# Kernel optimization log

Hardware: AMD Instinct MI355X
Metric: run time of the kernel (lower is better)

Reference implementation:

```python
import jax, jax.numpy as jnp
import numpy as np


def setup_inputs() -> dict:
    key = jax.random.key(0)
    ks = jax.random.split(key, 11)
    B, E, R, D = 2048, 20000, 500, 256
    inp = {
        "h": jax.random.uniform(ks[0], (B, E), dtype=jnp.float32),
        "t": jax.random.uniform(ks[1], (B, E), dtype=jnp.float32),
        "r": jax.random.uniform(ks[2], (B, R), dtype=jnp.float32),
        "W_er": jax.random.normal(ks[3], (D, E), dtype=jnp.float32) * 0.02,
        "W_ei": jax.random.normal(ks[4], (D, E), dtype=jnp.float32) * 0.02,
        "W_ej": jax.random.normal(ks[5], (D, E), dtype=jnp.float32) * 0.02,
        "W_ek": jax.random.normal(ks[6], (D, E), dtype=jnp.float32) * 0.02,
        "W_rr": jax.random.normal(ks[7], (D, R), dtype=jnp.float32) * 0.02,
        "W_ri": jax.random.normal(ks[8], (D, R), dtype=jnp.float32) * 0.02,
        "W_rj": jax.random.normal(ks[9], (D, R), dtype=jnp.float32) * 0.02,
        "W_rk": jax.random.normal(ks[10], (D, R), dtype=jnp.float32) * 0.02,
    }
    return inp


def reference(h, t, r, W_er, W_ei, W_ej, W_ek, W_rr, W_ri, W_rj, W_rk):
    # entity / relation projections (nn.Linear, no bias): x @ W^T -> [B, D]
    H_r, H_i, H_j, H_k = h @ W_er.T, h @ W_ei.T, h @ W_ej.T, h @ W_ek.T
    T_r, T_i, T_j, T_k = t @ W_er.T, t @ W_ei.T, t @ W_ej.T, t @ W_ek.T
    R_r, R_i, R_j, R_k = r @ W_rr.T, r @ W_ri.T, r @ W_rj.T, r @ W_rk.T

    # hypercomplex norm per row: sqrt(|R_r|^2 + |R_i|^2 + |R_j|^2 + |R_k|^2) -> [B,1]
    norm = jnp.sqrt(
        jnp.sum(R_r * R_r + R_i * R_i + R_j * R_j + R_k * R_k, axis=1, keepdims=True)
    )
    R_r, R_i, R_j, R_k = norm * R_r, norm * R_i, norm * R_j, norm * R_k

    # Hamilton product H (x) R
    Q_r = H_r * R_r - H_i * R_i - H_j * R_j - H_k * R_k
    Q_i = H_r * R_i + H_i * R_r + H_j * R_k - H_k * R_j
    Q_j = H_r * R_j - H_i * R_k + H_j * R_r + H_k * R_i
    Q_k = H_r * R_k + H_i * R_j - H_j * R_i + H_k * R_r

    # diag(Q @ T^T) == rowwise dot sum(Q*T, axis=1) -- O(B*d) form of the anti-pattern
    score = jnp.sum(Q_r * T_r + Q_i * T_i + Q_j * T_j + Q_k * T_k, axis=1, keepdims=True)
    return jax.nn.sigmoid(score)
```

## Files before the change

### kernel.cpp

```cpp
#include <hip/hip_runtime.h>


using bf16x8 = __attribute__((ext_vector_type(8))) short;
using f32x4  = __attribute__((ext_vector_type(4))) float;
using f32x16 = __attribute__((ext_vector_type(16))) float;

#define DEVINL static __device__ __forceinline__

DEVINL void split2(float x0, float x1, unsigned& h, unsigned& l) {
  unsigned u0 = __float_as_uint(x0), u1 = __float_as_uint(x1);
  unsigned h0 = u0 & 0xFFFF0000u, h1 = u1 & 0xFFFF0000u;
  h = (u0 >> 16) | h1;
  float r0 = x0 - __uint_as_float(h0);
  float r1 = x1 - __uint_as_float(h1);
  l = (__float_as_uint(r0) >> 16) | (__float_as_uint(r1) & 0xFFFF0000u);
}

DEVINL void gload16(const void* g, void* l) {
  __builtin_amdgcn_global_load_lds(
      (const __attribute__((address_space(1))) unsigned*)g,
      (__attribute__((address_space(3))) unsigned*)l, 16, 0, 0);
}

__global__ void convert_img128(const float* __restrict__ src0,
                               const float* __restrict__ src1, int rows0,
                               int srcK, char* __restrict__ dst, int ktiles)
{
  __shared__ float ld[64][36];
  const int kt = blockIdx.x, rb = blockIdx.y;
  const int t = threadIdx.x;

  {
    int r = t >> 2, kc = (t & 3) * 8;
    int row = rb * 64 + r;
    const float* srow = (row < rows0) ? (src0 + (size_t)row * srcK)
                                      : (src1 + (size_t)(row - rows0) * srcK);
    int k0 = kt * 32 + kc;
    float4 v0, v1;
    if (k0 + 8 <= srcK) {
      v0 = *(const float4*)(srow + k0);
      v1 = *(const float4*)(srow + k0 + 4);
    } else {
      float x[8];
#pragma unroll
      for (int j = 0; j < 8; ++j) x[j] = (k0 + j < srcK) ? srow[k0 + j] : 0.f;
      v0 = make_float4(x[0], x[1], x[2], x[3]);
      v1 = make_float4(x[4], x[5], x[6], x[7]);
    }
    *(float4*)&ld[r][kc]     = v0;
    *(float4*)&ld[r][kc + 4] = v1;
  }
  __syncthreads();

  {
    int g = t >> 7, s = (t >> 6) & 1, kh = (t >> 5) & 1, r31 = t & 31;
    int row = g * 32 + r31;
    int k = s * 16 + kh * 8;
    float x[8];
#pragma unroll
    for (int j = 0; j < 8; ++j) x[j] = ld[row][k + j];
    unsigned hh[4], llv[4];
    split2(x[0], x[1], hh[0], llv[0]);
    split2(x[2], x[3], hh[1], llv[1]);
    split2(x[4], x[5], hh[2], llv[2]);
    split2(x[6], x[7], hh[3], llv[3]);
    int tile_rt = rb >> 1;
    int gbase = (rb & 1) * 2;
    char* base = dst + ((size_t)tile_rt * ktiles + kt) * 16384
               + (gbase + g) * 2048 + s * 1024 + kh * 512 + r31 * 16;
    *(uint4*)base          = make_uint4(hh[0], hh[1], hh[2], hh[3]);
    *(uint4*)(base + 8192) = make_uint4(llv[0], llv[1], llv[2], llv[3]);
  }
}

__global__ __launch_bounds__(256, 2) void gemm_t128(
    const char* __restrict__ Aimg, const char* __restrict__ Bimg, int ktiles,
    float* __restrict__ C, int MT, int NT, int KS, int swz)
{
  __shared__ __align__(16) char smem[65536];
  const int bid = blockIdx.x;

  int mt, nt, ks;
  if (swz) {
    int x = bid & 7, i = bid >> 3;
    nt = i & 7;
    int P = x * 8 + (i >> 3);
    ks = P & 1; mt = P >> 1;
  } else {
    nt = bid % NT; int q = bid / NT; mt = q % MT; ks = q / MT;
  }

  const int kt0 = (ktiles * ks) / KS;
  const int kt1 = (ktiles * (ks + 1)) / KS;

  const char* Ab = Aimg + ((size_t)mt * ktiles + kt0) * 16384;
  const char* Bb = Bimg + ((size_t)nt * ktiles + kt0) * 16384;

  const int wid = threadIdx.x >> 6, lane = threadIdx.x & 63;
  const int wr = wid >> 1, wc = wid & 1;

  f32x16 acc[2][2];
#pragma unroll
  for (int mb = 0; mb < 2; ++mb)
#pragma unroll
    for (int nb = 0; nb < 2; ++nb)
#pragma unroll
      for (int e = 0; e < 16; ++e) acc[mb][nb][e] = 0.f;

  {
    const char* As = Ab + wid * 4096 + lane * 16;
    const char* Bs = Bb + wid * 4096 + lane * 16;
#pragma unroll
    for (int i = 0; i < 4; ++i) gload16(As + i * 1024, smem + wid * 4096 + i * 1024);
#pragma unroll
    for (int i = 0; i < 4; ++i) gload16(Bs + i * 1024, smem + 16384 + wid * 4096 + i * 1024);
  }
  asm volatile("s_waitcnt vmcnt(0)" ::: "memory");
  __builtin_amdgcn_s_barrier();

  for (int kt = kt0; kt < kt1; ++kt) {
    char* bufc = smem + (size_t)((kt - kt0) & 1) * 32768;
    char* bufn = smem + (size_t)(((kt - kt0) & 1) ^ 1) * 32768;
    const bool nx = (kt + 1 < kt1);

    if (nx) {
      const char* As = Ab + (size_t)(kt + 1 - kt0) * 16384 + wid * 4096 + lane * 16;
      const char* Bs = Bb + (size_t)(kt + 1 - kt0) * 16384 + wid * 4096 + lane * 16;
#pragma unroll
      for (int i = 0; i < 4; ++i) gload16(As + i * 1024, bufn + wid * 4096 + i * 1024);
#pragma unroll
      for (int i = 0; i < 4; ++i) gload16(Bs + i * 1024, bufn + 16384 + wid * 4096 + i * 1024);
    }

    bf16x8 ah[2][2], al[2][2], bh[2][2], bl[2][2];
#pragma unroll
    for (int mb = 0; mb < 2; ++mb)
#pragma unroll
      for (int s = 0; s < 2; ++s) {
        const char* p = bufc + (wr * 2 + mb) * 2048 + s * 1024 + lane * 16;
        ah[mb][s] = *(const bf16x8*)p;
        al[mb][s] = *(const bf16x8*)(p + 8192);
      }
#pragma unroll
    for (int nb = 0; nb < 2; ++nb)
#pragma unroll
      for (int s = 0; s < 2; ++s) {
        const char* p = bufc + 16384 + (wc * 2 + nb) * 2048 + s * 1024 + lane * 16;
        bh[nb][s] = *(const bf16x8*)p;
        bl[nb][s] = *(const bf16x8*)(p + 8192);
      }

    __builtin_amdgcn_s_setprio(1);
#pragma unroll
    for (int p = 0; p < 3; ++p)
#pragma unroll
      for (int s = 0; s < 2; ++s)
#pragma unroll
        for (int mb = 0; mb < 2; ++mb)
#pragma unroll
          for (int nb = 0; nb < 2; ++nb) {
            bf16x8 av = (p == 1) ? al[mb][s] : ah[mb][s];
            bf16x8 bv = (p == 2) ? bl[nb][s] : bh[nb][s];
            acc[mb][nb] = __builtin_amdgcn_mfma_f32_32x32x16_bf16(av, bv, acc[mb][nb], 0, 0, 0);
          }
    __builtin_amdgcn_s_setprio(0);

    asm volatile("s_waitcnt vmcnt(0)" ::: "memory");
    __builtin_amdgcn_s_barrier();
  }

  float* Cb = C + (size_t)ks * (size_t)(MT * 128) * 1024;
  const long rowbase = (long)mt * 128 + wr * 64 + 4 * (lane >> 5);
  const long colbase = (long)nt * 128 + wc * 64 + (lane & 31);
#pragma unroll
  for (int mb = 0; mb < 2; ++mb)
#pragma unroll
    for (int nb = 0; nb < 2; ++nb)
#pragma unroll
      for (int reg = 0; reg < 16; ++reg) {
        long row = rowbase + mb * 32 + (reg & 3) + 8 * (reg >> 2);
        long col = colbase + nb * 32;
        Cb[(size_t)row * 1024 + col] = acc[mb][nb][reg];
      }
}

__global__ void convert_b16(const float* __restrict__ src, int srcK,
                            char* __restrict__ dst)
{
  const int tile = blockIdx.x;
  const int wrow = threadIdx.x;
  char* base = dst + (size_t)tile * 32768;
  const float* srow = src + (size_t)wrow * srcK;
#pragma unroll
  for (int kc8 = 0; kc8 < 4; ++kc8) {
    int k0 = tile * 32 + kc8 * 8;
    float x[8];
    if (k0 + 8 <= srcK) {
      float4 v0 = *(const float4*)(srow + k0);
      float4 v1 = *(const float4*)(srow + k0 + 4);
      x[0] = v0.x; x[1] = v0.y; x[2] = v0.z; x[3] = v0.w;
      x[4] = v1.x; x[5] = v1.y; x[6] = v1.z; x[7] = v1.w;
    } else {
#pragma unroll
      for (int j = 0; j < 8; ++j) x[j] = (k0 + j < srcK) ? srow[k0 + j] : 0.f;
    }
    unsigned hh[4], ll[4];
    split2(x[0], x[1], hh[0], ll[0]);
    split2(x[2], x[3], hh[1], ll[1]);
    split2(x[4], x[5], hh[2], ll[2]);
    split2(x[6], x[7], hh[3], ll[3]);
    int lchunk = (wrow & 15) + kc8 * 16;
    int n16 = wrow >> 4;
    *(uint4*)(base + (size_t)n16 * 1024 + lchunk * 16)         = make_uint4(hh[0], hh[1], hh[2], hh[3]);
    *(uint4*)(base + 16384 + (size_t)n16 * 1024 + lchunk * 16) = make_uint4(ll[0], ll[1], ll[2], ll[3]);
  }
}

__global__ void pad_r(const float* __restrict__ src, float* __restrict__ dst)
{
  int row = blockIdx.y;
  int k = threadIdx.x * 4;
  float4 v = make_float4(0.f, 0.f, 0.f, 0.f);
  if (k + 3 < 500) v = *(const float4*)(src + (size_t)row * 500 + k);
  *(float4*)(dst + (size_t)row * 512 + k) = v;
}

__global__ __launch_bounds__(512, 2) void gemm3p(
    const float* __restrict__ A0, const float* __restrict__ A1, int mtA0, long lda,
    const char* __restrict__ Bimg, int ktilesTot,
    float* __restrict__ C, long ldc, int MT, int NT, int KS, int swz)
{
  extern __shared__ char smemd[];
  const int tid = threadIdx.x;
  const int bid = blockIdx.x;

  int mt, nt, ks;
  if (swz) {
    int x = bid & 7, w = bid >> 3;
    nt = w & 3;
    int g = x + (w >> 2) * 8;
    mt = g & 15; ks = g >> 4;
  } else {
    nt = bid % NT; int q = bid / NT; mt = q % MT; ks = q / MT;
  }

  const int kt0 = (ktilesTot * ks) / KS;
  const int kt1 = (ktilesTot * (ks + 1)) / KS;

  const float* Ablk = (mt < mtA0) ? (A0 + (size_t)mt * 256 * lda)
                                  : (A1 + (size_t)(mt - mtA0) * 256 * lda);
  const char* Bt = Bimg + ((size_t)nt * ktilesTot + kt0) * 32768;

  const int wid = tid >> 6, lane = tid & 63;
  const int wr = wid >> 2, wc = wid & 3;
  const int l15 = lane & 15, lq = lane >> 4;

  const float* aSrc = Ablk + (size_t)(wid * 32 + (lane >> 3)) * lda
                      + (size_t)kt0 * 32 + 4 * (lane & 7);

  int awoff[4];
  {
    int kg = (lane & 7) >> 1, half = lane & 1;
#pragma unroll
    for (int i = 0; i < 4; ++i) {
      int m15 = (lane >> 3) + 8 * (i & 1);
      awoff[i] = (2 * wid + (i >> 1)) * 2048 + (((m15 ^ kg) + kg * 16) << 4) + half * 8;
    }
  }
  const int aroff = (((l15 ^ lq) + lq * 16) << 4);
  const int bbase = 32768 + (wc * 4) * 1024 + lane * 16;

  f32x4 acc[8][4];
#pragma unroll
  for (int m = 0; m < 8; ++m)
#pragma unroll
    for (int j = 0; j < 4; ++j)
#pragma unroll
      for (int e = 0; e < 4; ++e) acc[m][j][e] = 0.f;

  float4 aR[4];

#define ISSUE_A(KT)                                                            \
  {                                                                            \
    const float* p_ = aSrc + (size_t)((KT) - kt0) * 32;                        \
    _Pragma("unroll")                                                          \
    for (int i = 0; i < 4; ++i) aR[i] = *(const float4*)(p_ + (size_t)(8 * i) * lda); \
  }
#define ISSUE_B(DST, KT)                                                       \
  {                                                                            \
    const char* p_ = Bt + (size_t)((KT) - kt0) * 32768 + wid * 4096 + lane * 16; \
    _Pragma("unroll")                                                          \
    for (int i = 0; i < 4; ++i)                                                \
      gload16(p_ + i * 1024, (DST) + 32768 + wid * 4096 + i * 1024);           \
  }
#define WRITE_A(DST)                                                           \
  {                                                                            \
    _Pragma("unroll")                                                          \
    for (int i = 0; i < 4; ++i) {                                              \
      unsigned h0_, l0_, h1_, l1_;                                             \
      split2(aR[i].x, aR[i].y, h0_, l0_);                                      \
      split2(aR[i].z, aR[i].w, h1_, l1_);                                      \
      *(uint2*)((DST) + awoff[i])        = make_uint2(h0_, h1_);               \
      *(uint2*)((DST) + awoff[i] + 1024) = make_uint2(l0_, l1_);               \
    }                                                                          \
  }

  ISSUE_A(kt0);
  ISSUE_B(smemd, kt0);
  WRITE_A(smemd);
  asm volatile("s_waitcnt vmcnt(0)" ::: "memory");
  asm volatile("s_waitcnt lgkmcnt(0)" ::: "memory");
  __builtin_amdgcn_s_barrier();

  for (int kt = kt0; kt < kt1; ++kt) {
    char* bufc = smemd + (size_t)((kt - kt0) & 1) * 65536;
    char* bufn = smemd + (size_t)(((kt - kt0) & 1) ^ 1) * 65536;
    const bool nx = (kt + 1 < kt1);

    if (nx) { ISSUE_A(kt + 1); ISSUE_B(bufn, kt + 1); }

    bf16x8 bh[4], bl[4];
#pragma unroll
    for (int j = 0; j < 4; ++j) {
      bh[j] = *(const bf16x8*)(bufc + bbase + j * 1024);
      bl[j] = *(const bf16x8*)(bufc + bbase + j * 1024 + 16384);
    }

    __builtin_amdgcn_s_setprio(1);
#pragma unroll
    for (int m = 0; m < 4; ++m) {
      const char* ab = bufc + (wr * 8 + m) * 2048;
      bf16x8 ah = *(const bf16x8*)(ab + aroff);
      bf16x8 al = *(const bf16x8*)(ab + aroff + 1024);
#pragma unroll
      for (int j = 0; j < 4; ++j) {
        acc[m][j] = __builtin_amdgcn_mfma_f32_16x16x32_bf16(ah, bh[j], acc[m][j], 0, 0, 0);
        acc[m][j] = __builtin_amdgcn_mfma_f32_16x16x32_bf16(al, bh[j], acc[m][j], 0, 0, 0);
        acc[m][j] = __builtin_amdgcn_mfma_f32_16x16x32_bf16(ah, bl[j], acc[m][j], 0, 0, 0);
      }
    }
    __builtin_amdgcn_s_setprio(0);

    __builtin_amdgcn_sched_barrier(0);
    if (nx) WRITE_A(bufn);

    __builtin_amdgcn_s_setprio(1);
#pragma unroll
    for (int m = 4; m < 8; ++m) {
      const char* ab = bufc + (wr * 8 + m) * 2048;
      bf16x8 ah = *(const bf16x8*)(ab + aroff);
      bf16x8 al = *(const bf16x8*)(ab + aroff + 1024);
#pragma unroll
      for (int j = 0; j < 4; ++j) {
        acc[m][j] = __builtin_amdgcn_mfma_f32_16x16x32_bf16(ah, bh[j], acc[m][j], 0, 0, 0);
        acc[m][j] = __builtin_amdgcn_mfma_f32_16x16x32_bf16(al, bh[j], acc[m][j], 0, 0, 0);
        acc[m][j] = __builtin_amdgcn_mfma_f32_16x16x32_bf16(ah, bl[j], acc[m][j], 0, 0, 0);
      }
    }
    __builtin_amdgcn_s_setprio(0);

    asm volatile("s_waitcnt vmcnt(0)" ::: "memory");
    asm volatile("s_waitcnt lgkmcnt(0)" ::: "memory");
    __builtin_amdgcn_s_barrier();
  }
#undef ISSUE_A
#undef ISSUE_B
#undef WRITE_A

  float* Cb = C + (size_t)ks * (size_t)(MT * 256) * (size_t)ldc;
  const long rowbase = (long)mt * 256 + wr * 128 + lq * 4;
  const long colbase = (long)nt * 256 + wc * 64 + l15;
#pragma unroll
  for (int m = 0; m < 8; ++m)
#pragma unroll
    for (int j = 0; j < 4; ++j)
#pragma unroll
      for (int reg = 0; reg < 4; ++reg) {
        long row = rowbase + m * 16 + reg;
        long col = colbase + j * 16;
        Cb[(size_t)row * ldc + col] = acc[m][j][reg];
      }
}

__global__ void epilogue_kernel(const float* __restrict__ C1, const float* __restrict__ C2,
                                float* __restrict__ out, int KS)
{
  const int b = blockIdx.x;
  const int d = threadIdx.x;
  const size_t SZ = 4096ull * 1024ull;

  float Hq[4], Tq[4], Rq[4];
#pragma unroll
  for (int q = 0; q < 4; ++q) {
    float hv = 0.f, tv = 0.f;
    for (int ks = 0; ks < KS; ++ks) {
      hv += C1[ks * SZ + (size_t)b * 1024 + q * 256 + d];
      tv += C1[ks * SZ + (size_t)(b + 2048) * 1024 + q * 256 + d];
    }
    Hq[q] = hv; Tq[q] = tv;
    Rq[q] = C2[(size_t)b * 1024 + q * 256 + d];
  }
  float nn = Rq[0]*Rq[0] + Rq[1]*Rq[1] + Rq[2]*Rq[2] + Rq[3]*Rq[3];
  float Qr = Hq[0]*Rq[0] - Hq[1]*Rq[1] - Hq[2]*Rq[2] - Hq[3]*Rq[3];
  float Qi = Hq[0]*Rq[1] + Hq[1]*Rq[0] + Hq[2]*Rq[3] - Hq[3]*Rq[2];
  float Qj = Hq[0]*Rq[2] - Hq[1]*Rq[3] + Hq[2]*Rq[0] + Hq[3]*Rq[1];
  float Qk = Hq[0]*Rq[3] + Hq[1]*Rq[2] - Hq[2]*Rq[1] + Hq[3]*Rq[0];
  float ss = Qr*Tq[0] + Qi*Tq[1] + Qj*Tq[2] + Qk*Tq[3];

#pragma unroll
  for (int o = 32; o; o >>= 1) {
    ss += __shfl_xor(ss, o);
    nn += __shfl_xor(nn, o);
  }
  __shared__ float red[8];
  int lane = d & 63, w = d >> 6;
  if (lane == 0) { red[w] = ss; red[4 + w] = nn; }
  __syncthreads();
  if (d == 0) {
    float S = red[0] + red[1] + red[2] + red[3];
    float N = red[4] + red[5] + red[6] + red[7];
    float score = sqrtf(N) * S;
    out[b] = 1.f / (1.f + expf(-score));
  }
}

extern "C" void kernel_launch(void* const* d_in, const int* in_sizes, int n_in,
                              void* d_out, int out_size, void* d_ws, size_t ws_size,
                              hipStream_t stream)
{
  const float* h = (const float*)d_in[0];
  const float* t = (const float*)d_in[1];
  const float* r = (const float*)d_in[2];
  const float* We[4] = {(const float*)d_in[3], (const float*)d_in[4],
                        (const float*)d_in[5], (const float*)d_in[6]};
  const float* Wr[4] = {(const float*)d_in[7], (const float*)d_in[8],
                        (const float*)d_in[9], (const float*)d_in[10]};
  float* out = (float*)d_out;
  char* ws = (char*)d_ws;

  const size_t offA  = 0;
  const size_t offB  = 327680000;
  const size_t offWr = offB + 81920000;
  const size_t offRi = offWr + 2097152;
  const size_t offC1 = offRi + 4194304;
  const size_t C1sz  = 4096ull * 1024ull * 4ull;
  const size_t offC2 = offC1 + 2 * C1sz;
  const size_t needImg = offC2 + 8388608;

  if (ws_size >= needImg) {
    float* C1 = (float*)(ws + offC1);
    float* C2 = (float*)(ws + offC2);

    convert_img128<<<dim3(625, 64), 256, 0, stream>>>(h, t, 2048, 20000, ws + offA, 625);
    for (int q = 0; q < 4; ++q) {
      convert_img128<<<dim3(625, 4), 256, 0, stream>>>(
          We[q], We[q], 2048, 20000, ws + offB + (size_t)q * 2 * 625 * 16384, 625);
      convert_img128<<<dim3(16, 4), 256, 0, stream>>>(
          Wr[q], Wr[q], 2048, 500, ws + offWr + (size_t)q * 2 * 16 * 16384, 16);
    }
    convert_img128<<<dim3(16, 32), 256, 0, stream>>>(r, r, 2048, 500, ws + offRi, 16);

    gemm_t128<<<dim3(512), 256, 0, stream>>>(
        ws + offA, ws + offB, 625, C1, 32, 8, 2, 1);
    gemm_t128<<<dim3(128), 256, 0, stream>>>(
        ws + offRi, ws + offWr, 16, C2, 16, 8, 1, 0);

    epilogue_kernel<<<dim3(2048), 256, 0, stream>>>(C1, C2, out, 2);
    return;
  }

  const size_t fB  = 0;
  const size_t fWr = 81920000;
  const size_t fR  = fWr + 2097152;
  const size_t fC1 = fR + 4194304;
  const int KS = (ws_size >= fC1 + 4 * C1sz + 8388608ull) ? 4 : 2;
  const size_t fC2 = fC1 + (size_t)KS * C1sz;

  float* rpad = (float*)(ws + fR);
  float* C1   = (float*)(ws + fC1);
  float* C2   = (float*)(ws + fC2);

  for (int q = 0; q < 4; ++q) {
    convert_b16<<<dim3(625), 256, 0, stream>>>(We[q], 20000, ws + fB + (size_t)q * 625 * 32768);
    convert_b16<<<dim3(16), 256, 0, stream>>>(Wr[q], 500, ws + fWr + (size_t)q * 16 * 32768);
  }
  pad_r<<<dim3(1, 2048), 128, 0, stream>>>(r, rpad);

  gemm3p<<<dim3(16 * 4 * KS), 512, 131072, stream>>>(
      h, t, 8, 20000L, (const char*)(ws + fB), 625,
      C1, 1024L, 16, 4, KS, KS == 4 ? 1 : 0);
  gemm3p<<<dim3(32), 512, 131072, stream>>>(
      rpad, rpad, 8, 512L, (const char*)(ws + fWr), 16,
      C2, 1024L, 8, 4, 1, 0);

  epilogue_kernel<<<dim3(2048), 256, 0, stream>>>(C1, C2, out, KS);
}
```

Measured before the change: 616.1 us.

## Enlarge GEMM block tile to 256x256 with split-K of four

The bf16 hi/lo split-precision GEMM now uses 256x256 output tiles per block instead of 128x128. Each wave holds a 4x4 grid of 32x32 accumulators and B fragments are double-buffered in registers across the nb loop. The packed image layout and the convert kernel change to match, and split-K goes from 2 to 4, giving 256 blocks. The larger tile raises arithmetic intensity and cuts global/LDS traffic per FLOP, at the cost of one block per CU (128KB LDS, many registers) and twice the partial-sum memory read back by the epilogue.

Result: slower. 633.8 us (+2.9%).

```diff
diff --git a/kernel.cpp b/kernel.cpp
--- a/kernel.cpp
+++ b/kernel.cpp
@@ -22,9 +22,9 @@
       (__attribute__((address_space(3))) unsigned*)l, 16, 0, 0);
 }
 
-__global__ void convert_img128(const float* __restrict__ src0,
-                               const float* __restrict__ src1, int rows0,
-                               int srcK, char* __restrict__ dst, int ktiles)
+__global__ void convert_img2(const float* __restrict__ src0,
+                             const float* __restrict__ src1, int rows0,
+                             int srcK, char* __restrict__ dst, int ktiles)
 {
   __shared__ float ld[64][36];
   const int kt = blockIdx.x, rb = blockIdx.y;
@@ -64,28 +64,28 @@
     split2(x[2], x[3], hh[1], llv[1]);
     split2(x[4], x[5], hh[2], llv[2]);
     split2(x[6], x[7], hh[3], llv[3]);
-    int tile_rt = rb >> 1;
-    int gbase = (rb & 1) * 2;
-    char* base = dst + ((size_t)tile_rt * ktiles + kt) * 16384
+    int tile_rt = rb >> 2;
+    int gbase = (rb & 3) * 2;
+    char* base = dst + ((size_t)tile_rt * ktiles + kt) * 32768
                + (gbase + g) * 2048 + s * 1024 + kh * 512 + r31 * 16;
-    *(uint4*)base          = make_uint4(hh[0], hh[1], hh[2], hh[3]);
-    *(uint4*)(base + 8192) = make_uint4(llv[0], llv[1], llv[2], llv[3]);
-  }
-}
-
-__global__ __launch_bounds__(256, 2) void gemm_t128(
+    *(uint4*)base           = make_uint4(hh[0], hh[1], hh[2], hh[3]);
+    *(uint4*)(base + 16384) = make_uint4(llv[0], llv[1], llv[2], llv[3]);
+  }
+}
+
+__global__ __launch_bounds__(256, 1) void gemm_fat(
     const char* __restrict__ Aimg, const char* __restrict__ Bimg, int ktiles,
     float* __restrict__ C, int MT, int NT, int KS, int swz)
 {
-  __shared__ __align__(16) char smem[65536];
+  __shared__ __align__(16) char smem[131072];
   const int bid = blockIdx.x;
 
   int mt, nt, ks;
   if (swz) {
-    int x = bid & 7, i = bid >> 3;
-    nt = i & 7;
-    int P = x * 8 + (i >> 3);
-    ks = P & 1; mt = P >> 1;
+    int x = bid & 7, w = bid >> 3;
+    nt = w & 3;
+    int g = x + (w >> 2) * 8;
+    mt = g & 15; ks = g >> 4;
   } else {
     nt = bid % NT; int q = bid / NT; mt = q % MT; ks = q / MT;
   }
@@ -93,89 +93,99 @@
   const int kt0 = (ktiles * ks) / KS;
   const int kt1 = (ktiles * (ks + 1)) / KS;
 
-  const char* Ab = Aimg + ((size_t)mt * ktiles + kt0) * 16384;
-  const char* Bb = Bimg + ((size_t)nt * ktiles + kt0) * 16384;
+  const char* Ab = Aimg + ((size_t)mt * ktiles + kt0) * 32768;
+  const char* Bb = Bimg + ((size_t)nt * ktiles + kt0) * 32768;
 
   const int wid = threadIdx.x >> 6, lane = threadIdx.x & 63;
   const int wr = wid >> 1, wc = wid & 1;
 
-  f32x16 acc[2][2];
-#pragma unroll
-  for (int mb = 0; mb < 2; ++mb)
-#pragma unroll
-    for (int nb = 0; nb < 2; ++nb)
+  f32x16 acc[4][4];
+#pragma unroll
+  for (int mb = 0; mb < 4; ++mb)
+#pragma unroll
+    for (int nb = 0; nb < 4; ++nb)
 #pragma unroll
       for (int e = 0; e < 16; ++e) acc[mb][nb][e] = 0.f;
 
-  {
-    const char* As = Ab + wid * 4096 + lane * 16;
-    const char* Bs = Bb + wid * 4096 + lane * 16;
-#pragma unroll
-    for (int i = 0; i < 4; ++i) gload16(As + i * 1024, smem + wid * 4096 + i * 1024);
-#pragma unroll
-    for (int i = 0; i < 4; ++i) gload16(Bs + i * 1024, smem + 16384 + wid * 4096 + i * 1024);
-  }
+  auto stage = [&](char* buf, size_t tOff) {
+    const char* src = (wid < 2) ? (Ab + tOff + (size_t)wid * 16384)
+                                : (Bb + tOff + (size_t)(wid - 2) * 16384);
+    char* dst = buf + wid * 16384;
+#pragma unroll
+    for (int i = 0; i < 16; ++i)
+      gload16(src + i * 1024 + lane * 16, dst + i * 1024);
+  };
+
+  stage(smem, 0);
   asm volatile("s_waitcnt vmcnt(0)" ::: "memory");
   __builtin_amdgcn_s_barrier();
 
+  const int abase = wr * 4 * 2048 + lane * 16;
+  const int bbase = 32768 + wc * 4 * 2048 + lane * 16;
+
   for (int kt = kt0; kt < kt1; ++kt) {
-    char* bufc = smem + (size_t)((kt - kt0) & 1) * 32768;
-    char* bufn = smem + (size_t)(((kt - kt0) & 1) ^ 1) * 32768;
+    char* bufc = smem + (size_t)((kt - kt0) & 1) * 65536;
+    char* bufn = smem + (size_t)(((kt - kt0) & 1) ^ 1) * 65536;
     const bool nx = (kt + 1 < kt1);
 
-    if (nx) {
-      const char* As = Ab + (size_t)(kt + 1 - kt0) * 16384 + wid * 4096 + lane * 16;
-      const char* Bs = Bb + (size_t)(kt + 1 - kt0) * 16384 + wid * 4096 + lane * 16;
-#pragma unroll
-      for (int i = 0; i < 4; ++i) gload16(As + i * 1024, bufn + wid * 4096 + i * 1024);
-#pragma unroll
-      for (int i = 0; i < 4; ++i) gload16(Bs + i * 1024, bufn + 16384 + wid * 4096 + i * 1024);
-    }
-
-    bf16x8 ah[2][2], al[2][2], bh[2][2], bl[2][2];
-#pragma unroll
-    for (int mb = 0; mb < 2; ++mb)
+    if (nx) stage(bufn, (size_t)(kt + 1 - kt0) * 32768);
+
+    bf16x8 ah[4][2], al[4][2];
+#pragma unroll
+    for (int mb = 0; mb < 4; ++mb)
 #pragma unroll
       for (int s = 0; s < 2; ++s) {
-        const char* p = bufc + (wr * 2 + mb) * 2048 + s * 1024 + lane * 16;
+        const char* p = bufc + abase + mb * 2048 + s * 1024;
         ah[mb][s] = *(const bf16x8*)p;
-        al[mb][s] = *(const bf16x8*)(p + 8192);
+        al[mb][s] = *(const bf16x8*)(p + 16384);
       }
-#pragma unroll
-    for (int nb = 0; nb < 2; ++nb)
-#pragma unroll
-      for (int s = 0; s < 2; ++s) {
-        const char* p = bufc + 16384 + (wc * 2 + nb) * 2048 + s * 1024 + lane * 16;
-        bh[nb][s] = *(const bf16x8*)p;
-        bl[nb][s] = *(const bf16x8*)(p + 8192);
+
+    bf16x8 bh[2][2], bl[2][2];
+#pragma unroll
+    for (int s = 0; s < 2; ++s) {
+      const char* p = bufc + bbase + s * 1024;
+      bh[0][s] = *(const bf16x8*)p;
+      bl[0][s] = *(const bf16x8*)(p + 16384);
+    }
+
+#pragma unroll
+    for (int nb = 0; nb < 4; ++nb) {
+      const int cur = nb & 1, nxt = cur ^ 1;
+      if (nb < 3) {
+#pragma unroll
+        for (int s = 0; s < 2; ++s) {
+          const char* p = bufc + bbase + (nb + 1) * 2048 + s * 1024;
+          bh[nxt][s] = *(const bf16x8*)p;
+          bl[nxt][s] = *(const bf16x8*)(p + 16384);
+        }
       }
-
-    __builtin_amdgcn_s_setprio(1);
-#pragma unroll
-    for (int p = 0; p < 3; ++p)
+      __builtin_amdgcn_sched_barrier(0);
+      __builtin_amdgcn_s_setprio(1);
 #pragma unroll
       for (int s = 0; s < 2; ++s)
 #pragma unroll
-        for (int mb = 0; mb < 2; ++mb)
-#pragma unroll
-          for (int nb = 0; nb < 2; ++nb) {
+        for (int p = 0; p < 3; ++p)
+#pragma unroll
+          for (int mb = 0; mb < 4; ++mb) {
             bf16x8 av = (p == 1) ? al[mb][s] : ah[mb][s];
-            bf16x8 bv = (p == 2) ? bl[nb][s] : bh[nb][s];
+            bf16x8 bv = (p == 2) ? bl[cur][s] : bh[cur][s];
             acc[mb][nb] = __builtin_amdgcn_mfma_f32_32x32x16_bf16(av, bv, acc[mb][nb], 0, 0, 0);
           }
-    __builtin_amdgcn_s_setprio(0);
+      __builtin_amdgcn_s_setprio(0);
+      __builtin_amdgcn_sched_barrier(0);
+    }
 
     asm volatile("s_waitcnt vmcnt(0)" ::: "memory");
     __builtin_amdgcn_s_barrier();
   }
 
-  float* Cb = C + (size_t)ks * (size_t)(MT * 128) * 1024;
-  const long rowbase = (long)mt * 128 + wr * 64 + 4 * (lane >> 5);
-  const long colbase = (long)nt * 128 + wc * 64 + (lane & 31);
-#pragma unroll
-  for (int mb = 0; mb < 2; ++mb)
-#pragma unroll
-    for (int nb = 0; nb < 2; ++nb)
+  float* Cb = C + (size_t)ks * (size_t)(MT * 256) * 1024;
+  const long rowbase = (long)mt * 256 + wr * 128 + 4 * (lane >> 5);
+  const long colbase = (long)nt * 256 + wc * 128 + (lane & 31);
+#pragma unroll
+  for (int mb = 0; mb < 4; ++mb)
+#pragma unroll
+    for (int nb = 0; nb < 4; ++nb)
 #pragma unroll
       for (int reg = 0; reg < 16; ++reg) {
         long row = rowbase + mb * 32 + (reg & 3) + 8 * (reg >> 2);
@@ -444,28 +454,28 @@
   const size_t offRi = offWr + 2097152;
   const size_t offC1 = offRi + 4194304;
   const size_t C1sz  = 4096ull * 1024ull * 4ull;
-  const size_t offC2 = offC1 + 2 * C1sz;
+  const size_t offC2 = offC1 + 4 * C1sz;
   const size_t needImg = offC2 + 8388608;
 
   if (ws_size >= needImg) {
     float* C1 = (float*)(ws + offC1);
     float* C2 = (float*)(ws + offC2);
 
-    convert_img128<<<dim3(625, 64), 256, 0, stream>>>(h, t, 2048, 20000, ws + offA, 625);
+    convert_img2<<<dim3(625, 64), 256, 0, stream>>>(h, t, 2048, 20000, ws + offA, 625);
     for (int q = 0; q < 4; ++q) {
-      convert_img128<<<dim3(625, 4), 256, 0, stream>>>(
-          We[q], We[q], 2048, 20000, ws + offB + (size_t)q * 2 * 625 * 16384, 625);
-      convert_img128<<<dim3(16, 4), 256, 0, stream>>>(
-          Wr[q], Wr[q], 2048, 500, ws + offWr + (size_t)q * 2 * 16 * 16384, 16);
-    }
-    convert_img128<<<dim3(16, 32), 256, 0, stream>>>(r, r, 2048, 500, ws + offRi, 16);
-
-    gemm_t128<<<dim3(512), 256, 0, stream>>>(
-        ws + offA, ws + offB, 625, C1, 32, 8, 2, 1);
-    gemm_t128<<<dim3(128), 256, 0, stream>>>(
-        ws + offRi, ws + offWr, 16, C2, 16, 8, 1, 0);
-
-    epilogue_kernel<<<dim3(2048), 256, 0, stream>>>(C1, C2, out, 2);
+      convert_img2<<<dim3(625, 4), 256, 0, stream>>>(
+          We[q], We[q], 2048, 20000, ws + offB + (size_t)q * 625 * 32768, 625);
+      convert_img2<<<dim3(16, 4), 256, 0, stream>>>(
+          Wr[q], Wr[q], 2048, 500, ws + offWr + (size_t)q * 16 * 32768, 16);
+    }
+    convert_img2<<<dim3(16, 32), 256, 0, stream>>>(r, r, 2048, 500, ws + offRi, 16);
+
+    gemm_fat<<<dim3(256), 256, 0, stream>>>(
+        ws + offA, ws + offB, 625, C1, 16, 4, 4, 1);
+    gemm_fat<<<dim3(32), 256, 0, stream>>>(
+        ws + offRi, ws + offWr, 16, C2, 8, 4, 1, 0);
+
+    epilogue_kernel<<<dim3(2048), 256, 0, stream>>>(C1, C2, out, 4);
     return;
   }
 
```
